# Performance work log

Measured on AMD Instinct MI355X. Metric: run time of the kernel, lower is better.

## Reference

```python
import jax, jax.numpy as jnp
import numpy as np

N_NODES = 50000
N_EDGES = 800000
IN_C, HID_C, OUT_C = 128, 64, 40


def setup_inputs() -> dict:
    key = jax.random.key(0)
    ks = jax.random.split(key, 8)
    x = jax.random.normal(ks[0], (N_NODES, IN_C), dtype=jnp.float32)
    edge_index = jax.random.randint(ks[1], (2, N_EDGES), 0, N_NODES, dtype=jnp.int32)
    # Glorot-style init for the three GCNConv linear layers (bias zero as in PyG default reset)
    def glorot(k, fan_in, fan_out):
        lim = jnp.sqrt(6.0 / (fan_in + fan_out)).astype(jnp.float32)
        return jax.random.uniform(k, (fan_in, fan_out), dtype=jnp.float32, minval=-lim, maxval=lim)
    return {
        "x": x,
        "edge_index": edge_index,
        "W1": glorot(ks[2], IN_C, HID_C), "b1": jnp.zeros((HID_C,), jnp.float32),
        "W2": glorot(ks[3], HID_C, HID_C), "b2": jnp.zeros((HID_C,), jnp.float32),
        "W3": glorot(ks[4], HID_C, OUT_C), "b3": jnp.zeros((OUT_C,), jnp.float32),
    }


def _gcn_norm(edge_index, num_nodes):
    # PyG gcn_norm: add self-loops (weight 1), symmetric D^-1/2 (A+I) D^-1/2.
    loop = jnp.arange(num_nodes, dtype=edge_index.dtype)
    row = jnp.concatenate([edge_index[0], loop])  # source
    col = jnp.concatenate([edge_index[1], loop])  # target
    w = jnp.ones(row.shape[0], dtype=jnp.float32)
    deg = jax.ops.segment_sum(w, col, num_segments=num_nodes)
    dinv = jnp.where(deg > 0, jax.lax.rsqrt(deg), 0.0)
    norm = dinv[row] * w * dinv[col]  # [E+N]
    return row, col, norm


def _gcn_conv(x, row, col, norm, W, b):
    h = x @ W                         # linear first, as in PyG GCNConv
    msg = h[row] * norm[:, None]      # gather + scale  [E+N, F]
    agg = jax.ops.segment_sum(msg, col, num_segments=x.shape[0])
    return agg + b


def reference(x, edge_index, W1, b1, W2, b2, W3, b3):
    row, col, norm = _gcn_norm(edge_index, x.shape[0])
    h = jax.nn.relu(_gcn_conv(x, row, col, norm, W1, b1))   # dropout: eval-mode identity
    h = jax.nn.relu(_gcn_conv(h, row, col, norm, W2, b2))
    h = _gcn_conv(h, row, col, norm, W3, b3)
    return jax.nn.log_softmax(h, axis=-1)
```

## Files before the change

### kernel.cpp

```cpp
#include <hip/hip_runtime.h>
#include <hip/hip_bf16.h>
#include <math.h>


#define BSHIFT 10
#define CHUNK 2048
#define CAP 24576

__global__ __launch_bounds__(64) void tinyzero_kernel(int* __restrict__ p) {
  p[threadIdx.x] = 0;
}


__global__ __launch_bounds__(256) void bucketA_kernel(const int* __restrict__ row,
                                                      const int* __restrict__ col,
                                                      int* __restrict__ bcursor,
                                                      int2* __restrict__ tmp, int e) {
  __shared__ int bcnt[64], bstart[64], bbase[64];
  __shared__ int2 stage[CHUNK];
  int tid = threadIdx.x;
  int base = blockIdx.x * CHUNK;
  int cnt = e - base;
  if (cnt > CHUNK) cnt = CHUNK;
  if (tid < 64) bcnt[tid] = 0;
  __syncthreads();

  int2 ed[CHUNK / 256];
  int rk[CHUNK / 256];
#pragma unroll
  for (int k = 0; k < CHUNK / 256; ++k) {
    int j = tid + k * 256;
    if (j < cnt) {
      int c = col[base + j], r = row[base + j];
      ed[k] = make_int2(c, r);
      rk[k] = atomicAdd(&bcnt[c >> BSHIFT], 1);
    }
  }
  __syncthreads();
  if (tid < 64) {
    int v = bcnt[tid];
    int run = v;
#pragma unroll
    for (int off = 1; off < 64; off <<= 1) {
      int t = __shfl_up(run, off);
      if (tid >= off) run += t;
    }
    bstart[tid] = run - v;
    if (v > 0) bbase[tid] = atomicAdd(&bcursor[tid], v);
  }
  __syncthreads();
#pragma unroll
  for (int k = 0; k < CHUNK / 256; ++k) {
    int j = tid + k * 256;
    if (j < cnt) stage[bstart[ed[k].x >> BSHIFT] + rk[k]] = ed[k];
  }
  __syncthreads();
  for (int s = tid; s < cnt; s += 256) {
    int2 ev = stage[s];
    int b = ev.x >> BSHIFT;
    tmp[(size_t)b * CAP + bbase[b] + (s - bstart[b])] = ev;
  }
}


__global__ __launch_bounds__(256) void scatterB_kernel(const int2* __restrict__ tmp,
                                                       const int* __restrict__ bcursor,
                                                       int4* __restrict__ meta,
                                                       float* __restrict__ dinv,
                                                       int* __restrict__ csr, int n) {
  __shared__ int cnt[1 << BSHIFT];
  __shared__ int part[256];
  int tid = threadIdx.x;
  int b = blockIdx.x;
  int node0 = b << BSHIFT;
  int m = bcursor[b];
  const int2* src = tmp + (size_t)b * CAP;

  for (int t = tid; t < (1 << BSHIFT); t += 256) cnt[t] = 0;
  __syncthreads();
  for (int i = tid; i < m; i += 256)
    atomicAdd(&cnt[src[i].x & ((1 << BSHIFT) - 1)], 1);
  __syncthreads();

  int c0 = cnt[tid * 4 + 0], c1 = cnt[tid * 4 + 1];
  int c2 = cnt[tid * 4 + 2], c3 = cnt[tid * 4 + 3];
  int lsum = c0 + c1 + c2 + c3;
  part[tid] = lsum;
  __syncthreads();
#pragma unroll
  for (int off = 1; off < 256; off <<= 1) {
    int t = (tid >= off) ? part[tid - off] : 0;
    __syncthreads();
    part[tid] += t;
    __syncthreads();
  }
  int e0 = (tid == 0 ? 0 : part[tid - 1]);
  int e1 = e0 + c0, e2 = e1 + c1, e3 = e2 + c2;
  int base = b * CAP;

  int nd = node0 + tid * 4;
  if (nd + 0 < n) { float d = rsqrtf((float)(c0 + 1)); meta[nd + 0] = make_int4(base + e0, c0, __float_as_int(d), 0); dinv[nd + 0] = d; }
  if (nd + 1 < n) { float d = rsqrtf((float)(c1 + 1)); meta[nd + 1] = make_int4(base + e1, c1, __float_as_int(d), 0); dinv[nd + 1] = d; }
  if (nd + 2 < n) { float d = rsqrtf((float)(c2 + 1)); meta[nd + 2] = make_int4(base + e2, c2, __float_as_int(d), 0); dinv[nd + 2] = d; }
  if (nd + 3 < n) { float d = rsqrtf((float)(c3 + 1)); meta[nd + 3] = make_int4(base + e3, c3, __float_as_int(d), 0); dinv[nd + 3] = d; }
  __syncthreads();
  cnt[tid * 4 + 0] = e0; cnt[tid * 4 + 1] = e1;
  cnt[tid * 4 + 2] = e2; cnt[tid * 4 + 3] = e3;
  __syncthreads();

  for (int i = tid; i < m; i += 256) {
    int2 ev = src[i];
    int pos = atomicAdd(&cnt[ev.x & ((1 << BSHIFT) - 1)], 1);
    csr[base + pos] = ev.y;
  }
}


template <int K, int F>
__global__ __launch_bounds__(256) void gemm_kernel(const float* __restrict__ X,
                                                   const float* __restrict__ W,
                                                   const float* __restrict__ dinv,
                                                   __hip_bfloat16* __restrict__ Y, int n) {
  __shared__ float xs[16][K];
  int tid = threadIdx.x;
  int node0 = blockIdx.x * 16;
  constexpr int KV = K / 4;
  const float4* X4 = (const float4*)X;
  for (int i = tid; i < 16 * KV; i += 256) {
    int r = i / KV, c = i % KV;
    int nd = node0 + r;
    float4 v = make_float4(0.f, 0.f, 0.f, 0.f);
    if (nd < n) v = X4[(size_t)nd * KV + c];
    ((float4*)&xs[r][0])[c] = v;
  }
  __syncthreads();
  int g = tid >> 6, lane = tid & 63;
  if (lane < F) {
    float acc0 = 0.f, acc1 = 0.f, acc2 = 0.f, acc3 = 0.f;
#pragma unroll 8
    for (int k = 0; k < K; ++k) {
      float w = W[k * F + lane];
      acc0 += xs[g * 4 + 0][k] * w;
      acc1 += xs[g * 4 + 1][k] * w;
      acc2 += xs[g * 4 + 2][k] * w;
      acc3 += xs[g * 4 + 3][k] * w;
    }
    float accs[4] = {acc0, acc1, acc2, acc3};
#pragma unroll
    for (int j = 0; j < 4; ++j) {
      int nd = node0 + g * 4 + j;
      if (nd < n) Y[(size_t)nd * F + lane] = __float2bfloat16(accs[j] * dinv[nd]);
    }
  }
}


__device__ __forceinline__ float bflo(unsigned int u) {
  return __uint_as_float(u << 16);
}
__device__ __forceinline__ float bfhi(unsigned int u) {
  return __uint_as_float(u & 0xffff0000u);
}

template <int F, int MODE>
__global__ __launch_bounds__(256) void agg_kernel(const unsigned short* __restrict__ Hs,
                                                  const int* __restrict__ csr,
                                                  const int4* __restrict__ meta,
                                                  const float* __restrict__ bias,
                                                  float* __restrict__ Y, int n) {
  constexpr int FP = F / 2;
  int wave = (blockIdx.x * 256 + threadIdx.x) >> 6;
  int lane = threadIdx.x & 63;
  if (wave >= n) return;
  int half = lane >> 5;
  int fid = lane & 31;
  bool activeF = (FP == 32) || (fid < FP);
  int4 mt = meta[wave];
  int s = mt.x, e = mt.x + mt.y;
  float di = __int_as_float(mt.z);

  float ax = 0.f, ay = 0.f;
  if (half == 0 && activeF) {
    unsigned int u = *(const unsigned int*)(Hs + (size_t)wave * F + 2 * fid);
    ax = bflo(u); ay = bfhi(u);
  }

  for (int base = s; base < e; base += 64) {
    int rem = e - base;
    int cnt = rem < 64 ? rem : 64;
    int p = csr[base + (lane < cnt ? lane : 0)];
    int j = 0;
    for (; j + 8 <= cnt; j += 8) {
      int r0 = __shfl(p, j + 0 + half);
      int r1 = __shfl(p, j + 2 + half);
      int r2 = __shfl(p, j + 4 + half);
      int r3 = __shfl(p, j + 6 + half);
      if (activeF) {
        unsigned int u0 = *(const unsigned int*)(Hs + (size_t)r0 * F + 2 * fid);
        unsigned int u1 = *(const unsigned int*)(Hs + (size_t)r1 * F + 2 * fid);
        unsigned int u2 = *(const unsigned int*)(Hs + (size_t)r2 * F + 2 * fid);
        unsigned int u3 = *(const unsigned int*)(Hs + (size_t)r3 * F + 2 * fid);
        ax += bflo(u0); ay += bfhi(u0);
        ax += bflo(u1); ay += bfhi(u1);
        ax += bflo(u2); ay += bfhi(u2);
        ax += bflo(u3); ay += bfhi(u3);
      }
    }
    for (; j < cnt; j += 2) {
      int idx = j + half;
      int r = __shfl(p, idx < cnt ? idx : j);
      if (activeF && idx < cnt) {
        unsigned int u = *(const unsigned int*)(Hs + (size_t)r * F + 2 * fid);
        ax += bflo(u); ay += bfhi(u);
      }
    }
  }

  ax += __shfl_xor(ax, 32);
  ay += __shfl_xor(ay, 32);

  if (MODE == 0) {
    if (half == 0 && activeF) {
      float b0 = bias[2 * fid], b1 = bias[2 * fid + 1];
      float v0 = ax * di + b0, v1 = ay * di + b1;
      v0 = v0 > 0.f ? v0 : 0.f;
      v1 = v1 > 0.f ? v1 : 0.f;
      *(float2*)(Y + (size_t)wave * F + 2 * fid) = make_float2(v0, v1);
    }
  } else {
    float b0 = activeF ? bias[2 * fid] : 0.f;
    float b1 = activeF ? bias[2 * fid + 1] : 0.f;
    float v0 = activeF ? ax * di + b0 : -INFINITY;
    float v1 = activeF ? ay * di + b1 : -INFINITY;
    float m = fmaxf(v0, v1);
#pragma unroll
    for (int off = 16; off; off >>= 1) m = fmaxf(m, __shfl_xor(m, off));
    float ex = (activeF ? expf(v0 - m) : 0.f) + (activeF ? expf(v1 - m) : 0.f);
#pragma unroll
    for (int off = 16; off; off >>= 1) ex += __shfl_xor(ex, off);
    float lg = logf(ex);
    if (half == 0 && activeF) {
      *(float2*)(Y + (size_t)wave * F + 2 * fid) =
          make_float2(v0 - m - lg, v1 - m - lg);
    }
  }
}


extern "C" void kernel_launch(void* const* d_in, const int* in_sizes, int n_in,
                              void* d_out, int out_size, void* d_ws, size_t ws_size,
                              hipStream_t stream) {
  const float* x  = (const float*)d_in[0];
  const int*   ei = (const int*)d_in[1];
  const float* W1 = (const float*)d_in[2];
  const float* b1 = (const float*)d_in[3];
  const float* W2 = (const float*)d_in[4];
  const float* b2 = (const float*)d_in[5];
  const float* W3 = (const float*)d_in[6];
  const float* b3 = (const float*)d_in[7];
  float* out = (float*)d_out;

  const int N = in_sizes[0] / 128;
  const int E = in_sizes[1] / 2;
  const int* erow = ei;
  const int* ecol = ei + E;

  const int nbuckets = (N + (1 << BSHIFT) - 1) >> BSHIFT;

  auto align_up = [](size_t v) { return (v + 255) & ~(size_t)255; };
  char* ws = (char*)d_ws;
  size_t off = 0;
  int* bcursor  = (int*)(ws + off); off += align_up(64 * 4);
  int4* meta    = (int4*)(ws + off); off += align_up((size_t)N * 16);
  float* dinv   = (float*)(ws + off); off += align_up((size_t)N * 4);
  int* csr      = (int*)(ws + off); off += align_up((size_t)nbuckets * CAP * 4);
  int2* tmp     = (int2*)(ws + off); off += align_up((size_t)nbuckets * CAP * 8);
  __hip_bfloat16* bufH = (__hip_bfloat16*)(ws + off); off += align_up((size_t)N * 64 * 2);
  float* bufF   = (float*)(ws + off); off += align_up((size_t)N * 64 * 4);
  (void)ws_size;

  const int cb = (E + CHUNK - 1) / CHUNK;

  tinyzero_kernel<<<1, 64, 0, stream>>>(bcursor);
  bucketA_kernel<<<cb, 256, 0, stream>>>(erow, ecol, bcursor, tmp, E);
  scatterB_kernel<<<nbuckets, 256, 0, stream>>>(tmp, bcursor, meta, dinv, csr, N);

  const int gemm_blocks = (N + 15) / 16;
  const int agg_blocks = (N + 3) / 4;

  gemm_kernel<128, 64><<<gemm_blocks, 256, 0, stream>>>(x, W1, dinv, bufH, N);
  agg_kernel<64, 0><<<agg_blocks, 256, 0, stream>>>((const unsigned short*)bufH, csr, meta, b1, bufF, N);

  gemm_kernel<64, 64><<<gemm_blocks, 256, 0, stream>>>(bufF, W2, dinv, bufH, N);
  agg_kernel<64, 0><<<agg_blocks, 256, 0, stream>>>((const unsigned short*)bufH, csr, meta, b2, bufF, N);

  gemm_kernel<64, 40><<<gemm_blocks, 256, 0, stream>>>(bufF, W3, dinv, bufH, N);
  agg_kernel<40, 1><<<agg_blocks, 256, 0, stream>>>((const unsigned short*)bufH, csr, meta, b3, out, N);
}
```

Measured before the change: 185.9 us.

## Process two nodes per wavefront with 8-byte bf16 gathers in aggregation

The aggregation kernel now assigns each half-wavefront (32 lanes) to its own node instead of one node per wave. Each lane gathers four bf16 features with a uint2 load, and two 16-lane subgroups split the neighbor list. This is meant to use the lanes better given about 17 neighbors per node, where a 64-lane wave with 2-byte-pair loads left much of each batch idle. It also widens the gathers, bias loads and stores. In exchange, each lane issues wider loads, and the log-softmax reductions shrink to 16-lane shuffles. The F=40 case leaves lanes 10-15 of each subgroup inactive.

Measured after the change: 168.8 us. -9.2%, faster.

```diff
diff --git a/kernel.cpp b/kernel.cpp
--- a/kernel.cpp
+++ b/kernel.cpp
@@ -168,80 +168,94 @@
                                                   const int4* __restrict__ meta,
                                                   const float* __restrict__ bias,
                                                   float* __restrict__ Y, int n) {
-  constexpr int FP = F / 2;
-  int wave = (blockIdx.x * 256 + threadIdx.x) >> 6;
+  constexpr int FQ = F / 4;
+  int wv = (blockIdx.x * 256 + threadIdx.x) >> 6;
   int lane = threadIdx.x & 63;
-  if (wave >= n) return;
   int half = lane >> 5;
-  int fid = lane & 31;
-  bool activeF = (FP == 32) || (fid < FP);
-  int4 mt = meta[wave];
+  int l32 = lane & 31;
+  int sub = l32 >> 4;
+  int fid = lane & 15;
+  int node = wv * 2 + half;
+  if (node >= n) return;
+  bool activeF = (FQ == 16) || (fid < FQ);
+  int hbase = 32 * half;
+
+  int4 mt = meta[node];
   int s = mt.x, e = mt.x + mt.y;
   float di = __int_as_float(mt.z);
 
-  float ax = 0.f, ay = 0.f;
-  if (half == 0 && activeF) {
-    unsigned int u = *(const unsigned int*)(Hs + (size_t)wave * F + 2 * fid);
-    ax = bflo(u); ay = bfhi(u);
-  }
-
-  for (int base = s; base < e; base += 64) {
+  float a0 = 0.f, a1 = 0.f, a2 = 0.f, a3 = 0.f;
+  if (sub == 0 && activeF) {
+    uint2 u = *(const uint2*)(Hs + (size_t)node * F + 4 * fid);
+    a0 = bflo(u.x); a1 = bfhi(u.x); a2 = bflo(u.y); a3 = bfhi(u.y);
+  }
+
+  for (int base = s; base < e; base += 32) {
     int rem = e - base;
-    int cnt = rem < 64 ? rem : 64;
-    int p = csr[base + (lane < cnt ? lane : 0)];
+    int cnt = rem < 32 ? rem : 32;
+    int p = csr[base + (l32 < cnt ? l32 : 0)];
     int j = 0;
     for (; j + 8 <= cnt; j += 8) {
-      int r0 = __shfl(p, j + 0 + half);
-      int r1 = __shfl(p, j + 2 + half);
-      int r2 = __shfl(p, j + 4 + half);
-      int r3 = __shfl(p, j + 6 + half);
+      int r0 = __shfl(p, j + 0 + sub + hbase);
+      int r1 = __shfl(p, j + 2 + sub + hbase);
+      int r2 = __shfl(p, j + 4 + sub + hbase);
+      int r3 = __shfl(p, j + 6 + sub + hbase);
       if (activeF) {
-        unsigned int u0 = *(const unsigned int*)(Hs + (size_t)r0 * F + 2 * fid);
-        unsigned int u1 = *(const unsigned int*)(Hs + (size_t)r1 * F + 2 * fid);
-        unsigned int u2 = *(const unsigned int*)(Hs + (size_t)r2 * F + 2 * fid);
-        unsigned int u3 = *(const unsigned int*)(Hs + (size_t)r3 * F + 2 * fid);
-        ax += bflo(u0); ay += bfhi(u0);
-        ax += bflo(u1); ay += bfhi(u1);
-        ax += bflo(u2); ay += bfhi(u2);
-        ax += bflo(u3); ay += bfhi(u3);
+        uint2 u0 = *(const uint2*)(Hs + (size_t)r0 * F + 4 * fid);
+        uint2 u1 = *(const uint2*)(Hs + (size_t)r1 * F + 4 * fid);
+        uint2 u2 = *(const uint2*)(Hs + (size_t)r2 * F + 4 * fid);
+        uint2 u3 = *(const uint2*)(Hs + (size_t)r3 * F + 4 * fid);
+        a0 += bflo(u0.x); a1 += bfhi(u0.x); a2 += bflo(u0.y); a3 += bfhi(u0.y);
+        a0 += bflo(u1.x); a1 += bfhi(u1.x); a2 += bflo(u1.y); a3 += bfhi(u1.y);
+        a0 += bflo(u2.x); a1 += bfhi(u2.x); a2 += bflo(u2.y); a3 += bfhi(u2.y);
+        a0 += bflo(u3.x); a1 += bfhi(u3.x); a2 += bflo(u3.y); a3 += bfhi(u3.y);
       }
     }
     for (; j < cnt; j += 2) {
-      int idx = j + half;
-      int r = __shfl(p, idx < cnt ? idx : j);
+      int idx = j + sub;
+      int r = __shfl(p, (idx < cnt ? idx : j) + hbase);
       if (activeF && idx < cnt) {
-        unsigned int u = *(const unsigned int*)(Hs + (size_t)r * F + 2 * fid);
-        ax += bflo(u); ay += bfhi(u);
+        uint2 u = *(const uint2*)(Hs + (size_t)r * F + 4 * fid);
+        a0 += bflo(u.x); a1 += bfhi(u.x); a2 += bflo(u.y); a3 += bfhi(u.y);
       }
     }
   }
 
-  ax += __shfl_xor(ax, 32);
-  ay += __shfl_xor(ay, 32);
+  a0 += __shfl_xor(a0, 16);
+  a1 += __shfl_xor(a1, 16);
+  a2 += __shfl_xor(a2, 16);
+  a3 += __shfl_xor(a3, 16);
 
   if (MODE == 0) {
-    if (half == 0 && activeF) {
-      float b0 = bias[2 * fid], b1 = bias[2 * fid + 1];
-      float v0 = ax * di + b0, v1 = ay * di + b1;
+    if (sub == 0 && activeF) {
+      float4 bv = *(const float4*)(bias + 4 * fid);
+      float v0 = a0 * di + bv.x, v1 = a1 * di + bv.y;
+      float v2 = a2 * di + bv.z, v3 = a3 * di + bv.w;
       v0 = v0 > 0.f ? v0 : 0.f;
       v1 = v1 > 0.f ? v1 : 0.f;
-      *(float2*)(Y + (size_t)wave * F + 2 * fid) = make_float2(v0, v1);
+      v2 = v2 > 0.f ? v2 : 0.f;
+      v3 = v3 > 0.f ? v3 : 0.f;
+      *(float4*)(Y + (size_t)node * F + 4 * fid) = make_float4(v0, v1, v2, v3);
     }
   } else {
-    float b0 = activeF ? bias[2 * fid] : 0.f;
-    float b1 = activeF ? bias[2 * fid + 1] : 0.f;
-    float v0 = activeF ? ax * di + b0 : -INFINITY;
-    float v1 = activeF ? ay * di + b1 : -INFINITY;
-    float m = fmaxf(v0, v1);
-#pragma unroll
-    for (int off = 16; off; off >>= 1) m = fmaxf(m, __shfl_xor(m, off));
-    float ex = (activeF ? expf(v0 - m) : 0.f) + (activeF ? expf(v1 - m) : 0.f);
-#pragma unroll
-    for (int off = 16; off; off >>= 1) ex += __shfl_xor(ex, off);
-    float lg = logf(ex);
-    if (half == 0 && activeF) {
-      *(float2*)(Y + (size_t)wave * F + 2 * fid) =
-          make_float2(v0 - m - lg, v1 - m - lg);
+    float v0 = -INFINITY, v1 = -INFINITY, v2 = -INFINITY, v3 = -INFINITY;
+    if (activeF) {
+      float4 bv = *(const float4*)(bias + 4 * fid);
+      v0 = a0 * di + bv.x; v1 = a1 * di + bv.y;
+      v2 = a2 * di + bv.z; v3 = a3 * di + bv.w;
+    }
+    float m = fmaxf(fmaxf(v0, v1), fmaxf(v2, v3));
+#pragma unroll
+    for (int off = 8; off; off >>= 1) m = fmaxf(m, __shfl_xor(m, off));
+    float ex = 0.f;
+    if (activeF)
+      ex = expf(v0 - m) + expf(v1 - m) + expf(v2 - m) + expf(v3 - m);
+#pragma unroll
+    for (int off = 8; off; off >>= 1) ex += __shfl_xor(ex, off);
+    float lg = m + logf(ex);
+    if (sub == 0 && activeF) {
+      *(float4*)(Y + (size_t)node * F + 4 * fid) =
+          make_float4(v0 - lg, v1 - lg, v2 - lg, v3 - lg);
     }
   }
 }
@@ -286,7 +300,7 @@
   scatterB_kernel<<<nbuckets, 256, 0, stream>>>(tmp, bcursor, meta, dinv, csr, N);
 
   const int gemm_blocks = (N + 15) / 16;
-  const int agg_blocks = (N + 3) / 4;
+  const int agg_blocks = (N + 7) / 8;
 
   gemm_kernel<128, 64><<<gemm_blocks, 256, 0, stream>>>(x, W1, dinv, bufH, N);
   agg_kernel<64, 0><<<agg_blocks, 256, 0, stream>>>((const unsigned short*)bufH, csr, meta, b1, bufF, N);
```
